# Optimization experiments

Measured on AMD Instinct MI355X. Metric: run time of the kernel, lower is better.

The kernel has to match this reference:

```python
import jax, jax.numpy as jnp
import numpy as np

N_NODES = 100000
N_EDGES = 1000000
D = 64
N_GRAPHS = 128
N_LAYERS = 3
BN_EPS = 1e-5


def setup_inputs() -> dict:
    key = jax.random.key(0)
    ks = jax.random.split(key, 8)
    x = jax.random.normal(ks[0], (N_NODES, D), dtype=jnp.float32)
    edge_index = jax.random.randint(ks[1], (2, N_EDGES), 0, N_NODES, dtype=jnp.int64)
    edge_attr = jax.random.uniform(ks[2], (N_EDGES,), dtype=jnp.float32)
    batch = jnp.sort(jax.random.randint(ks[3], (N_NODES,), 0, N_GRAPHS, dtype=jnp.int64))
    # xavier-uniform linear weights [L, out, in], zero conv bias (PyG GCNConv adds bias after aggregation)
    limit = float(np.sqrt(6.0 / (D + D)))
    W = jax.random.uniform(ks[4], (N_LAYERS, D, D), minval=-limit, maxval=limit, dtype=jnp.float32)
    b = jnp.zeros((N_LAYERS, D), dtype=jnp.float32)
    prelu_a = jnp.asarray(0.25, dtype=jnp.float32)  # single PReLU shared across layers
    bn_w = jnp.ones((N_LAYERS, D), dtype=jnp.float32)
    bn_b = jnp.zeros((N_LAYERS, D), dtype=jnp.float32)
    return {"x": x, "edge_index": edge_index, "edge_attr": edge_attr, "batch": batch,
            "W": W, "b": b, "prelu_a": prelu_a, "bn_w": bn_w, "bn_b": bn_b}


def reference(x, edge_index, edge_attr, batch, W, b, prelu_a, bn_w, bn_b):
    src, dst = edge_index[0], edge_index[1]
    h = x
    pooled = []
    for i in range(N_LAYERS):
        # GCNConv (normalize=False, add_self_loops=False): lin -> weighted scatter-add -> bias
        h = h @ W[i].T                                      # [N, D]
        msg = h[src] * edge_attr[:, None]                   # [E, D] gather + scale
        h = jax.ops.segment_sum(msg, dst, num_segments=N_NODES) + b[i]
        # shared PReLU
        h = jnp.where(h >= 0, h, prelu_a * h)
        # BatchNorm1d (training mode: biased batch stats over nodes)
        mean = jnp.mean(h, axis=0)
        var = jnp.mean((h - mean) ** 2, axis=0)
        h = (h - mean) * jax.lax.rsqrt(var + BN_EPS) * bn_w[i] + bn_b[i]
        pooled.append(jax.ops.segment_sum(h, batch, num_segments=N_GRAPHS))
    global_rep = jnp.concatenate(pooled, axis=1)            # [G, L*D]
    x_stack = pooled[-1]                                    # [G, D]
    return (global_rep, x_stack)
```

## Files before the change

kernel.cpp:

```cpp
#include <hip/hip_runtime.h>

#define NNODES 100000
#define NEDGES 1000000
#define DIM 64
#define NGRAPHS 128
#define NLAYERS 3
#define BN_EPS 1e-5f

#define BINSZ 8
#define NBINS 12500
#define GBLK 256
#define ECHUNK 3907
#define SLICES 4

#define OFF_EDGES   0
#define OFF_BINBASE 2000000
#define OFF_AGG     2012544
#define OFF_YBF     8412544
#define OFF_XBF     11612544
#define OFF_CNT     14812544
#define OFF_OFS     16412544
#define OFF_BTOT    18012544
#define OFF_GSUM4   18025088
#define OFF_PQ4     18057856
#define OFF_SCALE   18090624
#define OFF_SHIFT   18090816
#define OFF_END     18091008

__device__ __forceinline__ unsigned pack_bf16(float a, float b) {
    unsigned ua = __float_as_uint(a), ub = __float_as_uint(b);
    ua = (ua + 0x7FFFu + ((ua >> 16) & 1u)) >> 16;
    ub = (ub + 0x7FFFu + ((ub >> 16) & 1u)) & 0xFFFF0000u;
    return ua | ub;
}

__global__ __launch_bounds__(1024) void count_kernel(const int* __restrict__ ei,
                                                     const float* __restrict__ x,
                                                     const int* __restrict__ batch,
                                                     unsigned short* __restrict__ counts,
                                                     unsigned* __restrict__ xbf,
                                                     int* __restrict__ endv) {
    __shared__ int hist[NBINS];
    const int tid = threadIdx.x, blk = blockIdx.x;
    for (int i = tid; i < NBINS; i += 1024) hist[i] = 0;
    __syncthreads();
    const int e0 = blk * ECHUNK, e1 = min(NEDGES, e0 + ECHUNK);
    for (int e = e0 + tid; e < e1; e += 1024)
        atomicAdd(&hist[ei[NEDGES + e] >> 3], 1);
    __syncthreads();
    unsigned short* crow = counts + (size_t)blk * NBINS;
    for (int bin = tid; bin < NBINS; bin += 1024)
        crow[bin] = (unsigned short)hist[bin];
    const int gtid = blk * 1024 + tid;
    for (int i = gtid; i < NNODES * 32; i += GBLK * 1024) {
        const float2 v = *(const float2*)(x + (size_t)i * 2);
        xbf[i] = pack_bf16(v.x, v.y);
    }
    for (int i = gtid; i < NNODES; i += GBLK * 1024) {
        const int b0 = batch[i];
        const int b1 = (i + 1 < NNODES) ? batch[i + 1] : NGRAPHS;
        for (int g = b0; g < b1; ++g) endv[g] = i + 1;
        if (i == 0)
            for (int g = 0; g < b0; ++g) endv[g] = 0;
    }
}

__global__ __launch_bounds__(256) void s1_kernel(const unsigned short* __restrict__ counts,
                                                 unsigned short* __restrict__ offs,
                                                 int* __restrict__ btot) {
    const int bin = blockIdx.x * 256 + threadIdx.x;
    if (bin >= NBINS) return;
    int run = 0;
    for (int blk = 0; blk < GBLK; ++blk) {
        const int v = counts[(size_t)blk * NBINS + bin];
        offs[(size_t)blk * NBINS + bin] = (unsigned short)run;
        run += v;
    }
    btot[bin] = run;
}

__global__ __launch_bounds__(1024) void s2_kernel(const int* __restrict__ btot,
                                                  int* __restrict__ binBase) {
    __shared__ int wsum[16];
    const int t = threadIdx.x, wid = t >> 6, lane = t & 63;
    int running = 0;
    for (int b = 0; b < NBINS; b += 1024) {
        const int i = b + t;
        const int v = (i < NBINS) ? btot[i] : 0;
        int s = v;
        for (int off = 1; off < 64; off <<= 1) {
            int x = __shfl_up(s, off);
            if (lane >= off) s += x;
        }
        __syncthreads();
        if (lane == 63) wsum[wid] = s;
        __syncthreads();
        int pw = 0, tot = 0;
#pragma unroll
        for (int k = 0; k < 16; ++k) {
            const int x = wsum[k];
            tot += x;
            if (k < wid) pw += x;
        }
        if (i < NBINS) binBase[i] = running + pw + s - v;
        running += tot;
    }
    if (t == 0) binBase[NBINS] = running;
}

__global__ __launch_bounds__(1024) void scatter_kernel(const int* __restrict__ ei,
                                                       const float* __restrict__ ea,
                                                       const int* __restrict__ binBase,
                                                       const unsigned short* __restrict__ offs,
                                                       int2* __restrict__ edges) {
    __shared__ int cur[NBINS];
    const int tid = threadIdx.x, blk = blockIdx.x;
    const unsigned short* orow = offs + (size_t)blk * NBINS;
    for (int i = tid; i < NBINS; i += 1024)
        cur[i] = binBase[i] + (int)orow[i];
    __syncthreads();
    const int e0 = blk * ECHUNK, e1 = min(NEDGES, e0 + ECHUNK);
    for (int e = e0 + tid; e < e1; e += 1024) {
        const int dst = ei[NEDGES + e];
        const int src = ei[e];
        const float w = ea[e];
        const int pos = atomicAdd(&cur[dst >> 3], 1);
        edges[pos] = make_int2((src << 3) | (dst & (BINSZ - 1)), __float_as_int(w));
    }
}

template <bool FIRST>
__global__ __launch_bounds__(256) void agg_kernel(const unsigned* __restrict__ hbf,
                                                  const float* __restrict__ scale,
                                                  const float* __restrict__ shift,
                                                  const int* __restrict__ binBase,
                                                  const int2* __restrict__ edges,
                                                  float* __restrict__ agg) {
    __shared__ float accAll[4][2][BINSZ * 64];
    const int w = threadIdx.x >> 6, lane = threadIdx.x & 63;
    const int bin = blockIdx.x * 4 + w;
    const int half = lane >> 5, p = lane & 31, c0 = 2 * p;
    float* ac = accAll[w][half];
#pragma unroll
    for (int r = 0; r < BINSZ; ++r) *(float2*)&ac[r * 64 + c0] = make_float2(0.f, 0.f);
    float sc0 = 1.f, sc1 = 1.f, sh0 = 0.f, sh1 = 0.f;
    if (!FIRST) { sc0 = scale[c0]; sc1 = scale[c0 + 1]; sh0 = shift[c0]; sh1 = shift[c0 + 1]; }
    const int beg = binBase[bin], end = binBase[bin + 1];
    for (int j = beg; j < end; j += 64) {
        const int n = min(64, end - j);
        int2 ed = (j + lane < end) ? edges[j + lane] : make_int2(0, 0);
        const int n16 = n & ~15;
        int t = 0;
        for (; t < n16; t += 16) {
            int sd_[8]; float wt_[8]; unsigned u_[8];
#pragma unroll
            for (int q = 0; q < 8; ++q) {
                const int ii = t + 2 * q + half;
                sd_[q] = __shfl(ed.x, ii);
                wt_[q] = __int_as_float(__shfl(ed.y, ii));
            }
#pragma unroll
            for (int q = 0; q < 8; ++q) u_[q] = hbf[(size_t)(sd_[q] >> 3) * 32 + p];
#pragma unroll
            for (int q = 0; q < 8; ++q) {
                float h0 = __uint_as_float(u_[q] << 16);
                float h1 = __uint_as_float(u_[q] & 0xFFFF0000u);
                if (!FIRST) { h0 = fmaf(h0, sc0, sh0); h1 = fmaf(h1, sc1, sh1); }
                float2* a2 = (float2*)&ac[(sd_[q] & 7) * 64 + c0];
                float2 v = *a2;
                v.x = fmaf(wt_[q], h0, v.x);
                v.y = fmaf(wt_[q], h1, v.y);
                *a2 = v;
            }
        }
        for (; t < n; t += 2) {
            const int ii = min(t + half, n - 1);
            const int sd = __shfl(ed.x, ii);
            float wt = __int_as_float(__shfl(ed.y, ii));
            if (t + half >= n) wt = 0.f;
            const unsigned u = hbf[(size_t)(sd >> 3) * 32 + p];
            float h0 = __uint_as_float(u << 16);
            float h1 = __uint_as_float(u & 0xFFFF0000u);
            if (!FIRST) { h0 = fmaf(h0, sc0, sh0); h1 = fmaf(h1, sc1, sh1); }
            float2* a2 = (float2*)&ac[(sd & 7) * 64 + c0];
            float2 v = *a2;
            v.x = fmaf(wt, h0, v.x);
            v.y = fmaf(wt, h1, v.y);
            *a2 = v;
        }
    }
    const int nodeBase = bin * BINSZ;
#pragma unroll
    for (int r = 0; r < BINSZ; ++r)
        agg[(size_t)(nodeBase + r) * 64 + lane] =
            accAll[w][0][r * 64 + lane] + accAll[w][1][r * 64 + lane];
}

__global__ __launch_bounds__(256) void gemm_kernel(const float* __restrict__ agg,
                                                   const float* __restrict__ W,
                                                   const float* __restrict__ bias,
                                                   const float* __restrict__ pa_ptr,
                                                   unsigned* __restrict__ ybf) {
    __shared__ float As[128 * 68];
    __shared__ float Wt[64 * 68];
    const int tid = threadIdx.x;
    const int base = blockIdx.x * 128;
    for (int i = tid; i < 2048; i += 256) {
        const int r = i >> 4;
        const int q = (i & 15) * 4;
        const int row = base + r;
        float4 v = make_float4(0.f, 0.f, 0.f, 0.f);
        if (row < NNODES) v = *(const float4*)(agg + (size_t)row * 64 + q);
        *(float4*)&As[r * 68 + q] = v;
    }
    for (int i = tid; i < 4096; i += 256)
        Wt[(i & 63) * 68 + (i >> 6)] = W[i];
    __syncthreads();

    const int tc = tid & 7;
    const int tr = tid >> 3;
    float acc[4][8];
#pragma unroll
    for (int j = 0; j < 4; ++j)
#pragma unroll
        for (int c = 0; c < 8; ++c) acc[j][c] = 0.f;

    for (int kc = 0; kc < 16; ++kc) {
        const int k0 = kc * 4;
        float Af[4][4];
#pragma unroll
        for (int j = 0; j < 4; ++j) {
            const float4 t = *(const float4*)&As[(tr + 32 * j) * 68 + k0];
            Af[j][0] = t.x; Af[j][1] = t.y; Af[j][2] = t.z; Af[j][3] = t.w;
        }
#pragma unroll
        for (int kk = 0; kk < 4; ++kk) {
            const float4 w0 = *(const float4*)&Wt[(k0 + kk) * 68 + tc * 8];
            const float4 w1 = *(const float4*)&Wt[(k0 + kk) * 68 + tc * 8 + 4];
#pragma unroll
            for (int j = 0; j < 4; ++j) {
                const float a = Af[j][kk];
                acc[j][0] = fmaf(a, w0.x, acc[j][0]);
                acc[j][1] = fmaf(a, w0.y, acc[j][1]);
                acc[j][2] = fmaf(a, w0.z, acc[j][2]);
                acc[j][3] = fmaf(a, w0.w, acc[j][3]);
                acc[j][4] = fmaf(a, w1.x, acc[j][4]);
                acc[j][5] = fmaf(a, w1.y, acc[j][5]);
                acc[j][6] = fmaf(a, w1.z, acc[j][6]);
                acc[j][7] = fmaf(a, w1.w, acc[j][7]);
            }
        }
    }

    const float pa = *pa_ptr;
    const float4 b0 = *(const float4*)(bias + tc * 8);
    const float4 b1 = *(const float4*)(bias + tc * 8 + 4);
#pragma unroll
    for (int j = 0; j < 4; ++j) {
        const int row = base + tr + 32 * j;
        if (row >= NNODES) continue;
        float o[8];
        o[0] = acc[j][0] + b0.x; o[1] = acc[j][1] + b0.y;
        o[2] = acc[j][2] + b0.z; o[3] = acc[j][3] + b0.w;
        o[4] = acc[j][4] + b1.x; o[5] = acc[j][5] + b1.y;
        o[6] = acc[j][6] + b1.z; o[7] = acc[j][7] + b1.w;
#pragma unroll
        for (int c = 0; c < 8; ++c) o[c] = (o[c] >= 0.f) ? o[c] : pa * o[c];
        uint4 pk;
        pk.x = pack_bf16(o[0], o[1]);
        pk.y = pack_bf16(o[2], o[3]);
        pk.z = pack_bf16(o[4], o[5]);
        pk.w = pack_bf16(o[6], o[7]);
        *(uint4*)(ybf + (size_t)row * 32 + tc * 4) = pk;
    }
}

__global__ __launch_bounds__(256) void stats_kernel(const unsigned* __restrict__ ybf,
                                                    const int* __restrict__ endv,
                                                    float* __restrict__ gsum4,
                                                    float* __restrict__ pQ4) {
    __shared__ float red[2][8][64];
    const int g = blockIdx.x >> 2, s = blockIdx.x & 3;
    const int t = threadIdx.x, rl = t >> 5, p = t & 31, c0 = 2 * p;
    const int g0 = (g == 0) ? 0 : endv[g - 1];
    const int g1 = endv[g];
    const int len = g1 - g0;
    const int q0 = g0 + (len * s) / SLICES;
    const int q1 = g0 + (len * (s + 1)) / SLICES;
    float ga0 = 0.f, ga1 = 0.f, qq0 = 0.f, qq1 = 0.f;
    for (int r = q0 + rl; r < q1; r += 8) {
        const unsigned u = ybf[(size_t)r * 32 + p];
        const float f0 = __uint_as_float(u << 16);
        const float f1 = __uint_as_float(u & 0xFFFF0000u);
        ga0 += f0; ga1 += f1;
        qq0 = fmaf(f0, f0, qq0); qq1 = fmaf(f1, f1, qq1);
    }
    red[0][rl][c0] = ga0; red[0][rl][c0 + 1] = ga1;
    red[1][rl][c0] = qq0; red[1][rl][c0 + 1] = qq1;
    __syncthreads();
    if (rl == 0) {
        float a0 = 0.f, a1 = 0.f, b0 = 0.f, b1 = 0.f;
#pragma unroll
        for (int k = 0; k < 8; ++k) {
            a0 += red[0][k][c0]; a1 += red[0][k][c0 + 1];
            b0 += red[1][k][c0]; b1 += red[1][k][c0 + 1];
        }
        gsum4[blockIdx.x * 64 + c0] = a0; gsum4[blockIdx.x * 64 + c0 + 1] = a1;
        pQ4[blockIdx.x * 64 + c0] = b0;  pQ4[blockIdx.x * 64 + c0 + 1] = b1;
    }
}

__global__ __launch_bounds__(512) void finalize_kernel(const float* __restrict__ gsum4,
                                                       const float* __restrict__ pQ4,
                                                       const int* __restrict__ endv,
                                                       const float* __restrict__ bn_w,
                                                       const float* __restrict__ bn_b,
                                                       float* __restrict__ scale,
                                                       float* __restrict__ shift,
                                                       float* __restrict__ out, int layer) {
    __shared__ float rS[8][64], rQ[8][64];
    __shared__ float ssc[64], ssh[64];
    const int tid = threadIdx.x;
    const int c = tid & 63, pp = tid >> 6;
    float s = 0.f, q = 0.f;
    for (int sl = pp; sl < NGRAPHS * SLICES; sl += 8) {
        s += gsum4[sl * 64 + c];
        q += pQ4[sl * 64 + c];
    }
    rS[pp][c] = s; rQ[pp][c] = q;
    __syncthreads();
    if (tid < 64) {
        float S = 0.f, Q = 0.f;
#pragma unroll
        for (int k = 0; k < 8; ++k) { S += rS[k][c]; Q += rQ[k][c]; }
        const float mean = S * (1.f / NNODES);
        const float var = fmaxf(Q * (1.f / NNODES) - mean * mean, 0.f);
        const float inv = rsqrtf(var + BN_EPS);
        const float scv = inv * bn_w[c];
        const float shv = bn_b[c] - mean * scv;
        ssc[c] = scv; ssh[c] = shv;
        scale[c] = scv; shift[c] = shv;
    }
    __syncthreads();
    for (int idx = tid; idx < NGRAPHS * 64; idx += 512) {
        const int g = idx >> 6, ch = idx & 63;
        float gs = 0.f;
#pragma unroll
        for (int sl = 0; sl < SLICES; ++sl) gs += gsum4[(g * SLICES + sl) * 64 + ch];
        const int cnt = endv[g] - ((g == 0) ? 0 : endv[g - 1]);
        const float pooled = gs * ssc[ch] + (float)cnt * ssh[ch];
        out[g * (NLAYERS * 64) + layer * 64 + ch] = pooled;
        if (layer == NLAYERS - 1) out[NGRAPHS * NLAYERS * 64 + idx] = pooled;
    }
}

extern "C" void kernel_launch(void* const* d_in, const int* in_sizes, int n_in,
                              void* d_out, int out_size, void* d_ws, size_t ws_size,
                              hipStream_t stream) {
    const float* x     = (const float*)d_in[0];
    const int*   ei    = (const int*)d_in[1];
    const float* ea    = (const float*)d_in[2];
    const int*   batch = (const int*)d_in[3];
    const float* W     = (const float*)d_in[4];
    const float* b     = (const float*)d_in[5];
    const float* pa    = (const float*)d_in[6];
    const float* bn_w  = (const float*)d_in[7];
    const float* bn_b  = (const float*)d_in[8];
    float* out = (float*)d_out;
    float* ws  = (float*)d_ws;
    int*   wsi = (int*)d_ws;

    int2*           edges   = (int2*)(wsi + OFF_EDGES);
    int*            binBase = wsi + OFF_BINBASE;
    float*          agg     = ws + OFF_AGG;
    unsigned*       ybf     = (unsigned*)(wsi + OFF_YBF);
    unsigned*       xbf     = (unsigned*)(wsi + OFF_XBF);
    unsigned short* counts  = (unsigned short*)(wsi + OFF_CNT);
    unsigned short* offs    = (unsigned short*)(wsi + OFF_OFS);
    int*            btot    = wsi + OFF_BTOT;
    float*          gsum4   = ws + OFF_GSUM4;
    float*          pQ4     = ws + OFF_PQ4;
    float*          scaleA  = ws + OFF_SCALE;
    float*          shiftA  = ws + OFF_SHIFT;
    int*            endv    = wsi + OFF_END;

    count_kernel<<<GBLK, 1024, 0, stream>>>(ei, x, batch, counts, xbf, endv);
    s1_kernel<<<(NBINS + 255) / 256, 256, 0, stream>>>(counts, offs, btot);
    s2_kernel<<<1, 1024, 0, stream>>>(btot, binBase);
    scatter_kernel<<<GBLK, 1024, 0, stream>>>(ei, ea, binBase, offs, edges);

    for (int l = 0; l < NLAYERS; ++l) {
        if (l == 0)
            agg_kernel<true><<<NBINS / 4, 256, 0, stream>>>(xbf, nullptr, nullptr,
                                                            binBase, edges, agg);
        else
            agg_kernel<false><<<NBINS / 4, 256, 0, stream>>>(ybf, scaleA + (l - 1) * 64,
                                                             shiftA + (l - 1) * 64,
                                                             binBase, edges, agg);
        gemm_kernel<<<(NNODES + 127) / 128, 256, 0, stream>>>(agg, W + l * 4096, b + l * 64,
                                                              pa, ybf);
        stats_kernel<<<NGRAPHS * SLICES, 256, 0, stream>>>(ybf, endv, gsum4, pQ4);
        finalize_kernel<<<1, 512, 0, stream>>>(gsum4, pQ4, endv, bn_w + l * 64,
                                               bn_b + l * 64, scaleA + l * 64,
                                               shiftA + l * 64, out, l);
    }
}
```

Baseline: 309.6 us.

## Fuse aggregation with GEMM epilogue and merge stats with finalize via last-block

The per-layer aggregation now applies the 64x64 linear layer, bias and PReLU directly on the per-bin accumulators in shared memory and writes bf16 output. This removes the fp32 agg round trip through global memory and the separate GEMM launch. The BN stats and finalize kernels are merged using an atomic counter so the last block computes scale and shift. A ping-pong buffer is used because the fused kernel reads the previous layer's output while writing the new one. Weights are pre-transposed into float4 layout in the first kernel. The trade-off is a less efficient per-warp GEMM (each lane holds 8 rows and reads W from global/L2) and an extra fence and atomic per stats block.

```diff
diff --git a/kernel.cpp b/kernel.cpp
--- a/kernel.cpp
+++ b/kernel.cpp
@@ -15,17 +15,19 @@
 
 #define OFF_EDGES   0
 #define OFF_BINBASE 2000000
-#define OFF_AGG     2012544
-#define OFF_YBF     8412544
-#define OFF_XBF     11612544
-#define OFF_CNT     14812544
-#define OFF_OFS     16412544
-#define OFF_BTOT    18012544
-#define OFF_GSUM4   18025088
-#define OFF_PQ4     18057856
-#define OFF_SCALE   18090624
-#define OFF_SHIFT   18090816
-#define OFF_END     18091008
+#define OFF_YBFA    2012544
+#define OFF_YBFB    5212544
+#define OFF_XBF     8412544
+#define OFF_CNT     11612544
+#define OFF_OFS     13212544
+#define OFF_BTOT    14812544
+#define OFF_GSUM4   14825088
+#define OFF_PQ4     14857856
+#define OFF_SCALE   14890624
+#define OFF_SHIFT   14890816
+#define OFF_END     14891008
+#define OFF_WQ      14891136
+#define OFF_CTR     14903424
 
 __device__ __forceinline__ unsigned pack_bf16(float a, float b) {
     unsigned ua = __float_as_uint(a), ub = __float_as_uint(b);
@@ -37,9 +39,12 @@
 __global__ __launch_bounds__(1024) void count_kernel(const int* __restrict__ ei,
                                                      const float* __restrict__ x,
                                                      const int* __restrict__ batch,
+                                                     const float* __restrict__ W,
                                                      unsigned short* __restrict__ counts,
                                                      unsigned* __restrict__ xbf,
-                                                     int* __restrict__ endv) {
+                                                     int* __restrict__ endv,
+                                                     float4* __restrict__ wq,
+                                                     int* __restrict__ ctr) {
     __shared__ int hist[NBINS];
     const int tid = threadIdx.x, blk = blockIdx.x;
     for (int i = tid; i < NBINS; i += 1024) hist[i] = 0;
@@ -63,6 +68,11 @@
         if (i == 0)
             for (int g = 0; g < b0; ++g) endv[g] = 0;
     }
+    for (int i = gtid; i < NLAYERS * 1024; i += GBLK * 1024) {
+        const int l = i >> 10, rem = i & 1023, q = rem >> 6, c = rem & 63;
+        wq[i] = *(const float4*)(W + l * 4096 + c * 64 + q * 4);
+    }
+    if (gtid < NLAYERS) ctr[gtid] = 0;
 }
 
 __global__ __launch_bounds__(256) void s1_kernel(const unsigned short* __restrict__ counts,
@@ -130,12 +140,15 @@
 }
 
 template <bool FIRST>
-__global__ __launch_bounds__(256) void agg_kernel(const unsigned* __restrict__ hbf,
-                                                  const float* __restrict__ scale,
-                                                  const float* __restrict__ shift,
-                                                  const int* __restrict__ binBase,
-                                                  const int2* __restrict__ edges,
-                                                  float* __restrict__ agg) {
+__global__ __launch_bounds__(256) void agg_gemm_kernel(const unsigned* __restrict__ hbf,
+                                                       const float* __restrict__ scale,
+                                                       const float* __restrict__ shift,
+                                                       const int* __restrict__ binBase,
+                                                       const int2* __restrict__ edges,
+                                                       const float4* __restrict__ wq,
+                                                       const float* __restrict__ bias,
+                                                       const float* __restrict__ pa_ptr,
+                                                       unsigned* __restrict__ ybf) {
     __shared__ float accAll[4][2][BINSZ * 64];
     const int w = threadIdx.x >> 6, lane = threadIdx.x & 63;
     const int bin = blockIdx.x * 4 + w;
@@ -189,99 +202,57 @@
             *a2 = v;
         }
     }
+    float* ac0 = accAll[w][0];
+    float* ac1 = accAll[w][1];
+#pragma unroll
+    for (int r = 0; r < BINSZ; ++r)
+        ac0[r * 64 + lane] += ac1[r * 64 + lane];
+    const int c = lane;
+    const float bc = bias[c];
+    float o[BINSZ];
+#pragma unroll
+    for (int r = 0; r < BINSZ; ++r) o[r] = bc;
+    for (int q = 0; q < 16; ++q) {
+        const float4 wv = wq[q * 64 + c];
+#pragma unroll
+        for (int r = 0; r < BINSZ; ++r) {
+            const float4 a4 = *(const float4*)&ac0[r * 64 + q * 4];
+            o[r] = fmaf(a4.x, wv.x, o[r]);
+            o[r] = fmaf(a4.y, wv.y, o[r]);
+            o[r] = fmaf(a4.z, wv.z, o[r]);
+            o[r] = fmaf(a4.w, wv.w, o[r]);
+        }
+    }
+    const float pa = *pa_ptr;
+#pragma unroll
+    for (int r = 0; r < BINSZ; ++r) {
+        const float v = (o[r] >= 0.f) ? o[r] : pa * o[r];
+        ac1[r * 64 + c] = v;
+    }
     const int nodeBase = bin * BINSZ;
 #pragma unroll
-    for (int r = 0; r < BINSZ; ++r)
-        agg[(size_t)(nodeBase + r) * 64 + lane] =
-            accAll[w][0][r * 64 + lane] + accAll[w][1][r * 64 + lane];
-}
-
-__global__ __launch_bounds__(256) void gemm_kernel(const float* __restrict__ agg,
-                                                   const float* __restrict__ W,
-                                                   const float* __restrict__ bias,
-                                                   const float* __restrict__ pa_ptr,
-                                                   unsigned* __restrict__ ybf) {
-    __shared__ float As[128 * 68];
-    __shared__ float Wt[64 * 68];
-    const int tid = threadIdx.x;
-    const int base = blockIdx.x * 128;
-    for (int i = tid; i < 2048; i += 256) {
-        const int r = i >> 4;
-        const int q = (i & 15) * 4;
-        const int row = base + r;
-        float4 v = make_float4(0.f, 0.f, 0.f, 0.f);
-        if (row < NNODES) v = *(const float4*)(agg + (size_t)row * 64 + q);
-        *(float4*)&As[r * 68 + q] = v;
-    }
-    for (int i = tid; i < 4096; i += 256)
-        Wt[(i & 63) * 68 + (i >> 6)] = W[i];
-    __syncthreads();
-
-    const int tc = tid & 7;
-    const int tr = tid >> 3;
-    float acc[4][8];
-#pragma unroll
-    for (int j = 0; j < 4; ++j)
-#pragma unroll
-        for (int c = 0; c < 8; ++c) acc[j][c] = 0.f;
-
-    for (int kc = 0; kc < 16; ++kc) {
-        const int k0 = kc * 4;
-        float Af[4][4];
-#pragma unroll
-        for (int j = 0; j < 4; ++j) {
-            const float4 t = *(const float4*)&As[(tr + 32 * j) * 68 + k0];
-            Af[j][0] = t.x; Af[j][1] = t.y; Af[j][2] = t.z; Af[j][3] = t.w;
-        }
-#pragma unroll
-        for (int kk = 0; kk < 4; ++kk) {
-            const float4 w0 = *(const float4*)&Wt[(k0 + kk) * 68 + tc * 8];
-            const float4 w1 = *(const float4*)&Wt[(k0 + kk) * 68 + tc * 8 + 4];
-#pragma unroll
-            for (int j = 0; j < 4; ++j) {
-                const float a = Af[j][kk];
-                acc[j][0] = fmaf(a, w0.x, acc[j][0]);
-                acc[j][1] = fmaf(a, w0.y, acc[j][1]);
-                acc[j][2] = fmaf(a, w0.z, acc[j][2]);
-                acc[j][3] = fmaf(a, w0.w, acc[j][3]);
-                acc[j][4] = fmaf(a, w1.x, acc[j][4]);
-                acc[j][5] = fmaf(a, w1.y, acc[j][5]);
-                acc[j][6] = fmaf(a, w1.z, acc[j][6]);
-                acc[j][7] = fmaf(a, w1.w, acc[j][7]);
-            }
-        }
-    }
-
-    const float pa = *pa_ptr;
-    const float4 b0 = *(const float4*)(bias + tc * 8);
-    const float4 b1 = *(const float4*)(bias + tc * 8 + 4);
-#pragma unroll
-    for (int j = 0; j < 4; ++j) {
-        const int row = base + tr + 32 * j;
-        if (row >= NNODES) continue;
-        float o[8];
-        o[0] = acc[j][0] + b0.x; o[1] = acc[j][1] + b0.y;
-        o[2] = acc[j][2] + b0.z; o[3] = acc[j][3] + b0.w;
-        o[4] = acc[j][4] + b1.x; o[5] = acc[j][5] + b1.y;
-        o[6] = acc[j][6] + b1.z; o[7] = acc[j][7] + b1.w;
-#pragma unroll
-        for (int c = 0; c < 8; ++c) o[c] = (o[c] >= 0.f) ? o[c] : pa * o[c];
-        uint4 pk;
-        pk.x = pack_bf16(o[0], o[1]);
-        pk.y = pack_bf16(o[2], o[3]);
-        pk.z = pack_bf16(o[4], o[5]);
-        pk.w = pack_bf16(o[6], o[7]);
-        *(uint4*)(ybf + (size_t)row * 32 + tc * 4) = pk;
-    }
-}
-
-__global__ __launch_bounds__(256) void stats_kernel(const unsigned* __restrict__ ybf,
-                                                    const int* __restrict__ endv,
-                                                    float* __restrict__ gsum4,
-                                                    float* __restrict__ pQ4) {
+    for (int i = 0; i < 4; ++i) {
+        const int idx = lane + 64 * i;
+        const int r = idx >> 5, p2 = idx & 31;
+        ybf[(size_t)(nodeBase + r) * 32 + p2] =
+            pack_bf16(ac1[r * 64 + 2 * p2], ac1[r * 64 + 2 * p2 + 1]);
+    }
+}
+
+__global__ __launch_bounds__(256) void statsfin_kernel(const unsigned* __restrict__ ybf,
+                                                       const int* __restrict__ endv,
+                                                       float* __restrict__ gsum4,
+                                                       float* __restrict__ pQ4,
+                                                       const float* __restrict__ bn_w,
+                                                       const float* __restrict__ bn_b,
+                                                       float* __restrict__ scale,
+                                                       float* __restrict__ shift,
+                                                       float* __restrict__ out, int layer,
+                                                       int* __restrict__ ctr) {
     __shared__ float red[2][8][64];
+    __shared__ int amLast;
     const int g = blockIdx.x >> 2, s = blockIdx.x & 3;
-    const int t = threadIdx.x, rl = t >> 5, p = t & 31, c0 = 2 * p;
+    const int tid = threadIdx.x, rl = tid >> 5, p = tid & 31, c0 = 2 * p;
     const int g0 = (g == 0) ? 0 : endv[g - 1];
     const int g1 = endv[g];
     const int len = g1 - g0;
@@ -308,33 +279,27 @@
         gsum4[blockIdx.x * 64 + c0] = a0; gsum4[blockIdx.x * 64 + c0 + 1] = a1;
         pQ4[blockIdx.x * 64 + c0] = b0;  pQ4[blockIdx.x * 64 + c0 + 1] = b1;
     }
-}
-
-__global__ __launch_bounds__(512) void finalize_kernel(const float* __restrict__ gsum4,
-                                                       const float* __restrict__ pQ4,
-                                                       const int* __restrict__ endv,
-                                                       const float* __restrict__ bn_w,
-                                                       const float* __restrict__ bn_b,
-                                                       float* __restrict__ scale,
-                                                       float* __restrict__ shift,
-                                                       float* __restrict__ out, int layer) {
-    __shared__ float rS[8][64], rQ[8][64];
+    __threadfence();
+    if (tid == 0) amLast = (atomicAdd(ctr, 1) == NGRAPHS * SLICES - 1);
+    __syncthreads();
+    if (!amLast) return;
+    __threadfence();
+    __shared__ float rS[4][64], rQ[4][64];
     __shared__ float ssc[64], ssh[64];
-    const int tid = threadIdx.x;
     const int c = tid & 63, pp = tid >> 6;
-    float s = 0.f, q = 0.f;
-    for (int sl = pp; sl < NGRAPHS * SLICES; sl += 8) {
-        s += gsum4[sl * 64 + c];
-        q += pQ4[sl * 64 + c];
-    }
-    rS[pp][c] = s; rQ[pp][c] = q;
+    float S = 0.f, Q = 0.f;
+    for (int sl = pp; sl < NGRAPHS * SLICES; sl += 4) {
+        S += gsum4[sl * 64 + c];
+        Q += pQ4[sl * 64 + c];
+    }
+    rS[pp][c] = S; rQ[pp][c] = Q;
     __syncthreads();
     if (tid < 64) {
-        float S = 0.f, Q = 0.f;
-#pragma unroll
-        for (int k = 0; k < 8; ++k) { S += rS[k][c]; Q += rQ[k][c]; }
-        const float mean = S * (1.f / NNODES);
-        const float var = fmaxf(Q * (1.f / NNODES) - mean * mean, 0.f);
+        float SS = 0.f, QQ = 0.f;
+#pragma unroll
+        for (int k = 0; k < 4; ++k) { SS += rS[k][c]; QQ += rQ[k][c]; }
+        const float mean = SS * (1.f / NNODES);
+        const float var = fmaxf(QQ * (1.f / NNODES) - mean * mean, 0.f);
         const float inv = rsqrtf(var + BN_EPS);
         const float scv = inv * bn_w[c];
         const float shv = bn_b[c] - mean * scv;
@@ -342,14 +307,14 @@
         scale[c] = scv; shift[c] = shv;
     }
     __syncthreads();
-    for (int idx = tid; idx < NGRAPHS * 64; idx += 512) {
-        const int g = idx >> 6, ch = idx & 63;
+    for (int idx = tid; idx < NGRAPHS * 64; idx += 256) {
+        const int gg = idx >> 6, ch = idx & 63;
         float gs = 0.f;
 #pragma unroll
-        for (int sl = 0; sl < SLICES; ++sl) gs += gsum4[(g * SLICES + sl) * 64 + ch];
-        const int cnt = endv[g] - ((g == 0) ? 0 : endv[g - 1]);
+        for (int sl = 0; sl < SLICES; ++sl) gs += gsum4[(gg * SLICES + sl) * 64 + ch];
+        const int cnt = endv[gg] - ((gg == 0) ? 0 : endv[gg - 1]);
         const float pooled = gs * ssc[ch] + (float)cnt * ssh[ch];
-        out[g * (NLAYERS * 64) + layer * 64 + ch] = pooled;
+        out[gg * (NLAYERS * 64) + layer * 64 + ch] = pooled;
         if (layer == NLAYERS - 1) out[NGRAPHS * NLAYERS * 64 + idx] = pooled;
     }
 }
@@ -372,8 +337,8 @@
 
     int2*           edges   = (int2*)(wsi + OFF_EDGES);
     int*            binBase = wsi + OFF_BINBASE;
-    float*          agg     = ws + OFF_AGG;
-    unsigned*       ybf     = (unsigned*)(wsi + OFF_YBF);
+    unsigned*       ybfA    = (unsigned*)(wsi + OFF_YBFA);
+    unsigned*       ybfB    = (unsigned*)(wsi + OFF_YBFB);
     unsigned*       xbf     = (unsigned*)(wsi + OFF_XBF);
     unsigned short* counts  = (unsigned short*)(wsi + OFF_CNT);
     unsigned short* offs    = (unsigned short*)(wsi + OFF_OFS);
@@ -383,25 +348,27 @@
     float*          scaleA  = ws + OFF_SCALE;
     float*          shiftA  = ws + OFF_SHIFT;
     int*            endv    = wsi + OFF_END;
-
-    count_kernel<<<GBLK, 1024, 0, stream>>>(ei, x, batch, counts, xbf, endv);
+    float4*         wq      = (float4*)(ws + OFF_WQ);
+    int*            ctr     = wsi + OFF_CTR;
+
+    count_kernel<<<GBLK, 1024, 0, stream>>>(ei, x, batch, W, counts, xbf, endv, wq, ctr);
     s1_kernel<<<(NBINS + 255) / 256, 256, 0, stream>>>(counts, offs, btot);
     s2_kernel<<<1, 1024, 0, stream>>>(btot, binBase);
     scatter_kernel<<<GBLK, 1024, 0, stream>>>(ei, ea, binBase, offs, edges);
 
+    const unsigned* inb = xbf;
     for (int l = 0; l < NLAYERS; ++l) {
+        unsigned* outb = (l & 1) ? ybfB : ybfA;
         if (l == 0)
-            agg_kernel<true><<<NBINS / 4, 256, 0, stream>>>(xbf, nullptr, nullptr,
-                                                            binBase, edges, agg);
+            agg_gemm_kernel<true><<<NBINS / 4, 256, 0, stream>>>(
+                inb, nullptr, nullptr, binBase, edges, wq, b, pa, outb);
         else
-            agg_kernel<false><<<NBINS / 4, 256, 0, stream>>>(ybf, scaleA + (l - 1) * 64,
-                                                             shiftA + (l - 1) * 64,
-                                                             binBase, edges, agg);
-        gemm_kernel<<<(NNODES + 127) / 128, 256, 0, stream>>>(agg, W + l * 4096, b + l * 64,
-                                                              pa, ybf);
-        stats_kernel<<<NGRAPHS * SLICES, 256, 0, stream>>>(ybf, endv, gsum4, pQ4);
-        finalize_kernel<<<1, 512, 0, stream>>>(gsum4, pQ4, endv, bn_w + l * 64,
-                                               bn_b + l * 64, scaleA + l * 64,
-                                               shiftA + l * 64, out, l);
-    }
-}
+            agg_gemm_kernel<false><<<NBINS / 4, 256, 0, stream>>>(
+                inb, scaleA + (l - 1) * 64, shiftA + (l - 1) * 64, binBase, edges,
+                wq + (size_t)l * 1024, b + l * 64, pa, outb);
+        statsfin_kernel<<<NGRAPHS * SLICES, 256, 0, stream>>>(
+            outb, endv, gsum4, pQ4, bn_w + l * 64, bn_b + l * 64,
+            scaleA + l * 64, shiftA + l * 64, out, l, ctr + l);
+        inb = outb;
+    }
+}
```

Result: slower. 459.6 us (+48.4%).
